# Kernel optimization log

Measured on AMD Instinct MI355X. Metric: run time of the kernel, lower is better.

Reference implementation:

```python
import jax, jax.numpy as jnp
import numpy as np

H, NH, HD = 1024, 16, 64
B, T, S = 2, 1024, 3
NOISE, STEP, TEMP, NSTEPS = 0.1, 0.01, 1.0, 5
LN_EPS = 1e-5


def setup_inputs() -> dict:
    key = jax.random.key(0)
    ks = jax.random.split(key, 9)
    return {
        "queries": jax.random.normal(ks[0], (B, NH, T, HD), jnp.float32),
        "keys": jax.random.normal(ks[1], (B, NH, T, HD), jnp.float32),
        "values": jax.random.normal(ks[2], (B, NH, T, HD), jnp.float32),
        "hidden_states": jax.random.normal(ks[3], (B, T, H), jnp.float32),
        "W1": jax.random.normal(ks[4], (H, H), jnp.float32) * 0.02,
        "b1": jnp.zeros((H,), jnp.float32),
        "ln_g": jnp.ones((H,), jnp.float32),
        "ln_b": jnp.zeros((H,), jnp.float32),
        "W2": jax.random.normal(ks[5], (H, H), jnp.float32) * 0.02,
        "b2": jnp.zeros((H,), jnp.float32),
        "hyp_noise": jax.random.normal(ks[6], (S, B, NH, T, HD), jnp.float32),
        "ref_noise": jax.random.normal(ks[7], (S, NSTEPS - 1, B, NH, T, HD), jnp.float32),
    }


def _attention_energy(q, k, v):
    # q: [S,B,H,T,D]; k,v: [B,H,T,D] -> energy [S,B]
    scores = jnp.einsum('sbhtd,bhud->sbhtu', q, k) / jnp.sqrt(jnp.float32(q.shape[-1]))
    attn = jax.nn.softmax(scores, axis=-1)
    out = jnp.einsum('sbhtu,bhud->sbhtd', attn, v)
    out_mag = jnp.linalg.norm(out, axis=-1).mean(axis=(2, 3))          # [S,B]
    entropy = -(attn * jnp.log(attn + 1e-8)).sum(axis=-1).mean(axis=(2, 3))
    align = (q * k[None]).sum(axis=-1).mean(axis=(2, 3))
    return out_mag - 0.1 * entropy - 0.05 * align


def reference(queries, keys, values, hidden_states, W1, b1, ln_g, ln_b, W2, b2,
              hyp_noise, ref_noise):
    # query_predictor: Linear -> LayerNorm -> ReLU -> Linear
    x = hidden_states @ W1.T + b1
    mu = x.mean(axis=-1, keepdims=True)
    var = ((x - mu) ** 2).mean(axis=-1, keepdims=True)
    x = (x - mu) / jnp.sqrt(var + LN_EPS) * ln_g + ln_b
    x = jax.nn.relu(x)
    ctx = x @ W2.T + b2                                   # [B,T,H]
    ctx = ctx.reshape(B, T, NH, HD).transpose(0, 2, 1, 3) # [B,NH,T,HD]

    # exploration hypotheses, refined jointly over the sample axis
    q = queries[None] + hyp_noise * NOISE                 # [S,B,NH,T,HD]
    for step in range(NSTEPS):
        q = q - STEP * (q - ctx[None])                    # PCN prediction-error update
        if step < NSTEPS - 1:
            q = q + ref_noise[:, step] * 0.01

    energies = _attention_energy(q, keys, values)         # [S,B]
    probs = jax.nn.softmax(-energies / TEMP, axis=0)      # [S,B]
    selected = jnp.einsum('sb,sbhtd->bhtd', probs, q)     # softmax-weighted mix
    return selected, keys, values
```

## Files before the change

kernel.cpp:

```cpp
#include <hip/hip_runtime.h>
#include <hip/hip_bf16.h>
#include <math.h>

#define NB 2
#define NHH 16
#define TT 1024
#define HDD 64
#define NSS 3
#define HH 1024
#define MMR 2048

typedef float f4 __attribute__((ext_vector_type(4)));
typedef short bf16x8 __attribute__((ext_vector_type(8)));
typedef unsigned short u16;
typedef u16 u16x4 __attribute__((ext_vector_type(4)));

__device__ inline u16 f2bf(float f) {
    union { float f; unsigned u; } v; v.f = f;
    unsigned r = (v.u + 0x7FFFu + ((v.u >> 16) & 1u)) >> 16;
    return (u16)r;
}
__device__ inline float bf2f(u16 u) {
    union { unsigned u; float f; } v; v.u = ((unsigned)u) << 16;
    return v.f;
}

__device__ inline float red16sum(float v) {
    v += __shfl_xor(v, 1);
    v += __shfl_xor(v, 2);
    v += __shfl_xor(v, 4);
    v += __shfl_xor(v, 8);
    return v;
}
__device__ inline float red64sum(float v) {
    v += __shfl_xor(v, 1);
    v += __shfl_xor(v, 2);
    v += __shfl_xor(v, 4);
    v += __shfl_xor(v, 8);
    v += __shfl_xor(v, 16);
    v += __shfl_xor(v, 32);
    return v;
}

__global__ __launch_bounds__(256) void k_cvt4(const float* __restrict__ s0, u16* __restrict__ d0,
                                              const float* __restrict__ s1, u16* __restrict__ d1,
                                              const float* __restrict__ s2, u16* __restrict__ d2,
                                              const float* __restrict__ s3, u16* __restrict__ d3,
                                              float* __restrict__ outk) {
    int b = blockIdx.x;
    if (b >= 4096) {
        int i = (b - 4096) * 256 + threadIdx.x;
        f4 v = ((const f4*)s3)[i];
        ((f4*)outk)[i] = v;
        u16x4 o;
        o[0] = f2bf(v[0] * 0.125f); o[1] = f2bf(v[1] * 0.125f);
        o[2] = f2bf(v[2] * 0.125f); o[3] = f2bf(v[3] * 0.125f);
        ((u16x4*)d3)[i] = o;
        return;
    }
    const float* s; u16* d; int base;
    if (b < 2048)      { s = s0; d = d0; base = 0; }
    else if (b < 3072) { s = s1; d = d1; base = 2048; }
    else               { s = s2; d = d2; base = 3072; }
    int i = (b - base) * 256 + threadIdx.x;
    f4 v = ((const f4*)s)[i];
    u16x4 o;
    o[0] = f2bf(v[0]); o[1] = f2bf(v[1]); o[2] = f2bf(v[2]); o[3] = f2bf(v[3]);
    ((u16x4*)d)[i] = o;
}

__global__ __launch_bounds__(256) void k_vtrans(const float* __restrict__ V,
                                                u16* __restrict__ Vt,
                                                float* __restrict__ outv) {
    __shared__ float tile[64][65];
    int bh = blockIdx.y, t0 = blockIdx.x * 64;
    int r = threadIdx.x >> 2, c0 = (threadIdx.x & 3) * 16;
    const float* vp = V + ((size_t)bh * TT + t0) * HDD;
#pragma unroll
    for (int j = 0; j < 16; j += 4) {
        f4 v = *(const f4*)(vp + r * HDD + c0 + j);
        tile[r][c0 + j + 0] = v[0]; tile[r][c0 + j + 1] = v[1];
        tile[r][c0 + j + 2] = v[2]; tile[r][c0 + j + 3] = v[3];
        *(f4*)(outv + ((size_t)bh * TT + t0 + r) * HDD + c0 + j) = v;
    }
    __syncthreads();
    int d = threadIdx.x >> 2, x0 = (threadIdx.x & 3) * 16;
    u16* op = Vt + ((size_t)bh * HDD + d) * TT + t0 + x0;
#pragma unroll
    for (int j = 0; j < 16; j += 4) {
        u16x4 o;
        o[0] = f2bf(tile[x0 + j + 0][d]); o[1] = f2bf(tile[x0 + j + 1][d]);
        o[2] = f2bf(tile[x0 + j + 2][d]); o[3] = f2bf(tile[x0 + j + 3][d]);
        *(u16x4*)(op + j) = o;
    }
}

template <int EPI>
__global__ __launch_bounds__(256) void k_gemm_bt(const u16* __restrict__ A,
                                                 const u16* __restrict__ Bm,
                                                 const float* __restrict__ bias,
                                                 float* __restrict__ out) {
    const int K = 1024, N = 1024;
    int w = threadIdx.x >> 6, l = threadIdx.x & 63, lr = l & 15, lg = l >> 4;
    int m0 = blockIdx.y * 64 + w * 16;
    int n0 = blockIdx.x * 64;
    const u16* ap = A + (size_t)(m0 + lr) * K + lg * 8;
    const u16* bp = Bm + (size_t)(n0 + lr) * K + lg * 8;
    f4 z4 = {0.f, 0.f, 0.f, 0.f};
    f4 acc[4] = {z4, z4, z4, z4};
#pragma unroll 2
    for (int kk = 0; kk < K; kk += 32) {
        bf16x8 a  = *(const bf16x8*)(ap + kk);
        bf16x8 b0 = *(const bf16x8*)(bp + kk);
        bf16x8 b1 = *(const bf16x8*)(bp + 16 * K + kk);
        bf16x8 b2 = *(const bf16x8*)(bp + 32 * K + kk);
        bf16x8 b3 = *(const bf16x8*)(bp + 48 * K + kk);
        acc[0] = __builtin_amdgcn_mfma_f32_16x16x32_bf16(a, b0, acc[0], 0, 0, 0);
        acc[1] = __builtin_amdgcn_mfma_f32_16x16x32_bf16(a, b1, acc[1], 0, 0, 0);
        acc[2] = __builtin_amdgcn_mfma_f32_16x16x32_bf16(a, b2, acc[2], 0, 0, 0);
        acc[3] = __builtin_amdgcn_mfma_f32_16x16x32_bf16(a, b3, acc[3], 0, 0, 0);
    }
#pragma unroll
    for (int cf = 0; cf < 4; ++cf) {
        int col = n0 + cf * 16 + lr;
        float bs = bias[col];
#pragma unroll
        for (int r = 0; r < 4; ++r) {
            int row = m0 + lg * 4 + r;
            float v = acc[cf][r] + bs;
            if (EPI == 0) {
                out[(size_t)row * N + col] = v;
            } else {
                int b = row >> 10, t = row & 1023, nh = col >> 6, hd = col & 63;
                out[(((size_t)(b * NHH + nh)) * TT + t) * HDD + hd] = v;
            }
        }
    }
}

__global__ __launch_bounds__(256) void k_lnrelu(const float* __restrict__ X,
                                                const float* __restrict__ g,
                                                const float* __restrict__ bta,
                                                u16* __restrict__ xr) {
    int row = blockIdx.x;
    f4 v = ((const f4*)(X + (size_t)row * HH))[threadIdx.x];
    float s = v[0] + v[1] + v[2] + v[3];
    float s2 = v[0] * v[0] + v[1] * v[1] + v[2] * v[2] + v[3] * v[3];
    s = red64sum(s);
    s2 = red64sum(s2);
    __shared__ float red[8];
    int w = threadIdx.x >> 6, l = threadIdx.x & 63;
    if (l == 0) { red[w] = s; red[w + 4] = s2; }
    __syncthreads();
    float S1 = red[0] + red[1] + red[2] + red[3];
    float S2 = red[4] + red[5] + red[6] + red[7];
    float mu = S1 * (1.0f / 1024.0f);
    float var = S2 * (1.0f / 1024.0f) - mu * mu;
    float rstd = rsqrtf(var + 1e-5f);
    f4 gv = ((const f4*)g)[threadIdx.x];
    f4 bv = ((const f4*)bta)[threadIdx.x];
    u16x4 o;
#pragma unroll
    for (int j = 0; j < 4; ++j) {
        float y = (v[j] - mu) * rstd * gv[j] + bv[j];
        y = fmaxf(y, 0.f);
        o[j] = f2bf(y);
    }
    ((u16x4*)(xr + (size_t)row * HH))[threadIdx.x] = o;
}

__global__ __launch_bounds__(256, 3) void k_attn(const float* __restrict__ que,
                                                 const float* __restrict__ ctx,
                                                 const float* __restrict__ hyp,
                                                 const float* __restrict__ rn,
                                                 const u16* __restrict__ Kb,
                                                 const u16* __restrict__ Vt,
                                                 u16* __restrict__ qq,
                                                 float* __restrict__ part) {
    int bi = blockIdx.x;
    int qt2 = bi & 7, h = (bi >> 3) & 15, sb = bi >> 7;
    int s = sb >> 1, b = sb & 1;
    int bh = b * NHH + h;
    int w = threadIdx.x >> 6, l = threadIdx.x & 63, lr = l & 15, lg = l >> 4;
    int t0 = qt2 * 128;
    f4 z4 = {0.f, 0.f, 0.f, 0.f};

    __shared__ u16 Ks[4096];
    __shared__ u16 Vs[4096];
    __shared__ u16 plds[8][1024];

    const float A5 = 0.9509900499f, CC = 1.0f - A5, CH = 0.1f * A5;
    const float C0 = 0.0096059601f, C1 = 0.0097029900f, C2 = 0.0098010000f, C3 = 0.0099f;
    const float* quep = que + ((size_t)bh * TT) * HDD;
    const float* ctxp = ctx + ((size_t)bh * TT) * HDD;
    const float* hypp = hyp + ((size_t)(sb * NHH + h) * TT) * HDD;
    const float* rn0p = rn + ((size_t)(((s * 4 + 0) * 2 + b) * NHH + h) * TT) * HDD;
    const float* rn1p = rn + ((size_t)(((s * 4 + 1) * 2 + b) * NHH + h) * TT) * HDD;
    const float* rn2p = rn + ((size_t)(((s * 4 + 2) * 2 + b) * NHH + h) * TT) * HDD;
    const float* rn3p = rn + ((size_t)(((s * 4 + 3) * 2 + b) * NHH + h) * TT) * HDD;
    u16* qqp = qq + ((size_t)(sb * NHH + h) * TT) * HDD;

    bf16x8 aq[2][2];
#pragma unroll
    for (int qr = 0; qr < 2; ++qr) {
        size_t ro = (size_t)(t0 + w * 32 + qr * 16 + lr) * HDD;
#pragma unroll
        for (int c = 0; c < 2; ++c) {
            int d0 = c * 32 + lg * 8;
            f4 va, vb;
#pragma unroll
            for (int half = 0; half < 2; ++half) {
                size_t off = ro + d0 + half * 4;
                f4 v = A5 * *(const f4*)(quep + off);
                v += CC * *(const f4*)(ctxp + off);
                v += CH * __builtin_nontemporal_load((const f4*)(hypp + off));
                v += C0 * __builtin_nontemporal_load((const f4*)(rn0p + off));
                v += C1 * __builtin_nontemporal_load((const f4*)(rn1p + off));
                v += C2 * __builtin_nontemporal_load((const f4*)(rn2p + off));
                v += C3 * __builtin_nontemporal_load((const f4*)(rn3p + off));
                if (half == 0) va = v; else vb = v;
            }
            union { bf16x8 f; u16 u[8]; int4 i4; } o;
#pragma unroll
            for (int j = 0; j < 4; ++j) { o.u[j] = f2bf(va[j]); o.u[4 + j] = f2bf(vb[j]); }
            aq[qr][c] = o.f;
            *(int4*)(qqp + ro + d0) = o.i4;
        }
    }

    const u16* kbase = Kb + (size_t)bh * TT * HDD;
    const u16* vbase = Vt + (size_t)bh * HDD * TT;
    int u0 = threadIdx.x, u1 = threadIdx.x + 256;
    const u16* kg0 = kbase + u0 * 8;
    const u16* kg1 = kbase + u1 * 8;
    const u16* vg0 = vbase + (size_t)(u0 >> 3) * TT + (u0 & 7) * 8;
    const u16* vg1 = vbase + (size_t)(u1 >> 3) * TT + (u1 & 7) * 8;
    int ko0 = (u0 >> 3) * 128 + (((u0 & 7) ^ ((u0 >> 3) & 7)) << 4);
    int ko1 = (u1 >> 3) * 128 + (((u1 & 7) ^ ((u1 >> 3) & 7)) << 4);
    char* KsB = (char*)Ks;
    char* VsB = (char*)Vs;

    int4 kr0 = *(const int4*)(kg0);
    int4 kr1 = *(const int4*)(kg1);
    int4 vr0 = *(const int4*)(vg0);
    int4 vr1 = *(const int4*)(vg1);

    f4 acco[2][4] = {{z4, z4, z4, z4}, {z4, z4, z4, z4}};
    float zrow[2][4] = {{0.f, 0.f, 0.f, 0.f}, {0.f, 0.f, 0.f, 0.f}};
    float wrow[2][4] = {{0.f, 0.f, 0.f, 0.f}, {0.f, 0.f, 0.f, 0.f}};

    for (int kt = 0; kt < 16; ++kt) {
        __syncthreads();
        *(int4*)(KsB + ko0) = kr0;
        *(int4*)(KsB + ko1) = kr1;
        *(int4*)(VsB + ko0) = vr0;
        *(int4*)(VsB + ko1) = vr1;
        if (kt < 15) {
            kr0 = *(const int4*)(kg0 + (kt + 1) * 4096);
            kr1 = *(const int4*)(kg1 + (kt + 1) * 4096);
            vr0 = *(const int4*)(vg0 + (kt + 1) * 64);
            vr1 = *(const int4*)(vg1 + (kt + 1) * 64);
        }
        __syncthreads();

        f4 sc[2][4];
#pragma unroll
        for (int cf = 0; cf < 4; ++cf) {
            int row = cf * 16 + lr, rs = row & 7;
            bf16x8 bk0 = *(const bf16x8*)(KsB + row * 128 + ((lg ^ rs) << 4));
            bf16x8 bk1 = *(const bf16x8*)(KsB + row * 128 + (((4 + lg) ^ rs) << 4));
            f4 t0a = __builtin_amdgcn_mfma_f32_16x16x32_bf16(aq[0][0], bk0, z4, 0, 0, 0);
            sc[0][cf] = __builtin_amdgcn_mfma_f32_16x16x32_bf16(aq[0][1], bk1, t0a, 0, 0, 0);
            f4 t1a = __builtin_amdgcn_mfma_f32_16x16x32_bf16(aq[1][0], bk0, z4, 0, 0, 0);
            sc[1][cf] = __builtin_amdgcn_mfma_f32_16x16x32_bf16(aq[1][1], bk1, t1a, 0, 0, 0);
        }

#pragma unroll
        for (int qr = 0; qr < 2; ++qr) {
            u16* pl = &plds[w * 2 + qr][0];
#pragma unroll
            for (int cf = 0; cf < 4; ++cf) {
#pragma unroll
                for (int r = 0; r < 4; ++r) {
                    float sv = sc[qr][cf][r];
                    float pe = __expf(sv);
                    zrow[qr][r] += pe;
                    wrow[qr][r] = fmaf(pe, sv, wrow[qr][r]);
                    int prow = lg * 4 + r;
                    pl[(prow * 64 + cf * 16 + lr) ^ ((prow & 7) << 3)] = f2bf(pe);
                }
            }
        }
        bf16x8 pa[2][2];
#pragma unroll
        for (int qr = 0; qr < 2; ++qr) {
            const u16* pl = &plds[w * 2 + qr][0];
            pa[qr][0] = *(const bf16x8*)&pl[(lr * 64 + lg * 8) ^ ((lr & 7) << 3)];
            pa[qr][1] = *(const bf16x8*)&pl[(lr * 64 + 32 + lg * 8) ^ ((lr & 7) << 3)];
        }
#pragma unroll
        for (int cf = 0; cf < 4; ++cf) {
            int row = cf * 16 + lr, rs = row & 7;
            bf16x8 bv0 = *(const bf16x8*)(VsB + row * 128 + ((lg ^ rs) << 4));
            bf16x8 bv1 = *(const bf16x8*)(VsB + row * 128 + (((4 + lg) ^ rs) << 4));
            acco[0][cf] = __builtin_amdgcn_mfma_f32_16x16x32_bf16(pa[0][0], bv0, acco[0][cf], 0, 0, 0);
            acco[0][cf] = __builtin_amdgcn_mfma_f32_16x16x32_bf16(pa[0][1], bv1, acco[0][cf], 0, 0, 0);
            acco[1][cf] = __builtin_amdgcn_mfma_f32_16x16x32_bf16(pa[1][0], bv0, acco[1][cf], 0, 0, 0);
            acco[1][cf] = __builtin_amdgcn_mfma_f32_16x16x32_bf16(pa[1][1], bv1, acco[1][cf], 0, 0, 0);
        }
    }

    float magw = 0.f, entw = 0.f;
#pragma unroll
    for (int qr = 0; qr < 2; ++qr) {
#pragma unroll
        for (int r = 0; r < 4; ++r) {
            float zz = red16sum(zrow[qr][r]);
            float ww = red16sum(wrow[qr][r]);
            float ssq = acco[qr][0][r] * acco[qr][0][r] + acco[qr][1][r] * acco[qr][1][r] +
                        acco[qr][2][r] * acco[qr][2][r] + acco[qr][3][r] * acco[qr][3][r];
            ssq = red16sum(ssq);
            float inv = 1.0f / zz;
            magw += sqrtf(ssq) * inv;
            entw += __logf(zz) - ww * inv;
        }
    }
    magw += __shfl_xor(magw, 16); magw += __shfl_xor(magw, 32);
    entw += __shfl_xor(entw, 16); entw += __shfl_xor(entw, 32);

    int arow = threadIdx.x >> 1, ah = (threadIdx.x & 1) * 32;
    const u16* qa = qqp + (size_t)(t0 + arow) * HDD + ah;
    const u16* ka = Kb + (((size_t)bh) * TT + t0 + arow) * HDD + ah;
    float al = 0.f;
#pragma unroll
    for (int j = 0; j < 32; j += 4) {
        u16x4 qv4 = *(const u16x4*)(qa + j);
        u16x4 kv4 = *(const u16x4*)(ka + j);
        al += bf2f(qv4[0]) * bf2f(kv4[0]) + bf2f(qv4[1]) * bf2f(kv4[1]) +
              bf2f(qv4[2]) * bf2f(kv4[2]) + bf2f(qv4[3]) * bf2f(kv4[3]);
    }
    al = red64sum(al) * 8.0f;

    __shared__ float red[4][3];
    if (l == 0) { red[w][0] = magw; red[w][1] = entw; red[w][2] = al; }
    __syncthreads();
    if (threadIdx.x == 0) {
        part[bi * 3 + 0] = red[0][0] + red[1][0] + red[2][0] + red[3][0];
        part[bi * 3 + 1] = red[0][1] + red[1][1] + red[2][1] + red[3][1];
        part[bi * 3 + 2] = red[0][2] + red[1][2] + red[2][2] + red[3][2];
    }
}

__global__ void k_finalize(const float* __restrict__ part, float* __restrict__ probs) {
    int w = threadIdx.x >> 6, l = threadIdx.x & 63;
    __shared__ float eng[6];
    if (w < 6) {
        float a0 = 0.f, a1 = 0.f, a2 = 0.f;
        for (int i = l; i < 128; i += 64) {
            const float* pp = part + (size_t)(w * 128 + i) * 3;
            a0 += pp[0]; a1 += pp[1]; a2 += pp[2];
        }
        a0 = red64sum(a0); a1 = red64sum(a1); a2 = red64sum(a2);
        if (l == 0) {
            const float inv = 1.0f / 16384.0f;
            eng[w] = a0 * inv - 0.1f * (a1 * inv) - 0.05f * (a2 * inv);
        }
    }
    __syncthreads();
    if (threadIdx.x < 2) {
        int b = threadIdx.x;
        float e0 = -eng[0 + b], e1 = -eng[2 + b], e2 = -eng[4 + b];
        float mx = fmaxf(e0, fmaxf(e1, e2));
        float x0 = __expf(e0 - mx), x1 = __expf(e1 - mx), x2 = __expf(e2 - mx);
        float inv = 1.0f / (x0 + x1 + x2);
        probs[0 + b] = x0 * inv;
        probs[2 + b] = x1 * inv;
        probs[4 + b] = x2 * inv;
    }
}

__global__ __launch_bounds__(256) void k_select(const u16* __restrict__ qq,
                                                const float* __restrict__ probs,
                                                float* __restrict__ out) {
    const int NQ4 = 524288;
    int i = blockIdx.x * 256 + threadIdx.x;
    int b = i >> 18;
    float p0 = probs[0 + b], p1 = probs[2 + b], p2 = probs[4 + b];
    u16x4 a0 = ((const u16x4*)qq)[i];
    u16x4 a1 = ((const u16x4*)qq)[NQ4 + i];
    u16x4 a2 = ((const u16x4*)qq)[2 * NQ4 + i];
    f4 v;
#pragma unroll
    for (int j = 0; j < 4; ++j)
        v[j] = p0 * bf2f(a0[j]) + p1 * bf2f(a1[j]) + p2 * bf2f(a2[j]);
    ((f4*)out)[i] = v;
}

extern "C" void kernel_launch(void* const* d_in, const int* in_sizes, int n_in,
                              void* d_out, int out_size, void* d_ws, size_t ws_size,
                              hipStream_t stream) {
    const float* queries = (const float*)d_in[0];
    const float* keys    = (const float*)d_in[1];
    const float* values  = (const float*)d_in[2];
    const float* hs      = (const float*)d_in[3];
    const float* W1      = (const float*)d_in[4];
    const float* b1      = (const float*)d_in[5];
    const float* ln_g    = (const float*)d_in[6];
    const float* ln_b    = (const float*)d_in[7];
    const float* W2      = (const float*)d_in[8];
    const float* b2      = (const float*)d_in[9];
    const float* hyp     = (const float*)d_in[10];
    const float* rn      = (const float*)d_in[11];
    float* out = (float*)d_out;
    char* ws = (char*)d_ws;

    const size_t MB = 1024ull * 1024ull;
    u16*   qq16 = (u16*)(ws);
    u16*   hs_b = (u16*)(ws + 0 * MB);
    u16*   w1_b = (u16*)(ws + 4 * MB);
    u16*   w2_b = (u16*)(ws + 6 * MB);
    float* X    = (float*)(ws + 8 * MB);
    u16*   xr   = (u16*)(ws + 16 * MB);
    float* ctx  = (float*)(ws + 24 * MB);
    u16*   k_b  = (u16*)(ws + 32 * MB);
    u16*   vt_b = (u16*)(ws + 36 * MB);
    float* part = (float*)(ws + 40 * MB);
    float* probs= (float*)(ws + 40 * MB + 65536);

    k_cvt4<<<6144, 256, 0, stream>>>(hs, hs_b, W1, w1_b, W2, w2_b, keys, k_b,
                                     out + 2097152);
    k_vtrans<<<dim3(16, 32), 256, 0, stream>>>(values, vt_b, out + 4194304);

    k_gemm_bt<0><<<dim3(16, 32), 256, 0, stream>>>(hs_b, w1_b, b1, X);
    k_lnrelu<<<2048, 256, 0, stream>>>(X, ln_g, ln_b, xr);
    k_gemm_bt<1><<<dim3(16, 32), 256, 0, stream>>>(xr, w2_b, b2, ctx);

    k_attn<<<768, 256, 0, stream>>>(queries, ctx, hyp, rn, k_b, vt_b, qq16, part);
    k_finalize<<<1, 384, 0, stream>>>(part, probs);
    k_select<<<2048, 256, 0, stream>>>(qq16, probs, out);
}
```

Measured before the change: 175.7 us.

## Compute transposed scores and repack P via cross-lane shuffles instead of LDS

The QK^T MFMA now swaps its operands so each lane holds scores for one query row across several keys. The exp'd probabilities are packed to bf16 with v_cvt_pk_bf16_f32 and rearranged into the PV A-operand layout with two rounds of __shfl_xor, replacing the per-warp LDS scratch round trip and freeing 16KB of shared memory. The per-row softmax sums are accumulated per lane and reduced once at the end, with the reduction logic adjusted to match. This removes LDS writes and reads and scalar bf16 conversions, at the cost of extra cross-lane shuffles and selects per tile.

After: 183.3 us. 1.04x slower.

```diff
diff --git a/kernel.cpp b/kernel.cpp
--- a/kernel.cpp
+++ b/kernel.cpp
@@ -182,12 +182,12 @@
     int s = sb >> 1, b = sb & 1;
     int bh = b * NHH + h;
     int w = threadIdx.x >> 6, l = threadIdx.x & 63, lr = l & 15, lg = l >> 4;
+    int b4 = (l >> 4) & 1, b5 = (l >> 5) & 1;
     int t0 = qt2 * 128;
     f4 z4 = {0.f, 0.f, 0.f, 0.f};
 
     __shared__ u16 Ks[4096];
     __shared__ u16 Vs[4096];
-    __shared__ u16 plds[8][1024];
 
     const float A5 = 0.9509900499f, CC = 1.0f - A5, CH = 0.1f * A5;
     const float C0 = 0.0096059601f, C1 = 0.0097029900f, C2 = 0.0098010000f, C3 = 0.0099f;
@@ -246,8 +246,8 @@
     int4 vr1 = *(const int4*)(vg1);
 
     f4 acco[2][4] = {{z4, z4, z4, z4}, {z4, z4, z4, z4}};
-    float zrow[2][4] = {{0.f, 0.f, 0.f, 0.f}, {0.f, 0.f, 0.f, 0.f}};
-    float wrow[2][4] = {{0.f, 0.f, 0.f, 0.f}, {0.f, 0.f, 0.f, 0.f}};
+    float zacc[2] = {0.f, 0.f};
+    float wacc[2] = {0.f, 0.f};
 
     for (int kt = 0; kt < 16; ++kt) {
         __syncthreads();
@@ -263,41 +263,64 @@
         }
         __syncthreads();
 
-        f4 sc[2][4];
+        f4 st[2][4];
 #pragma unroll
         for (int cf = 0; cf < 4; ++cf) {
             int row = cf * 16 + lr, rs = row & 7;
             bf16x8 bk0 = *(const bf16x8*)(KsB + row * 128 + ((lg ^ rs) << 4));
             bf16x8 bk1 = *(const bf16x8*)(KsB + row * 128 + (((4 + lg) ^ rs) << 4));
-            f4 t0a = __builtin_amdgcn_mfma_f32_16x16x32_bf16(aq[0][0], bk0, z4, 0, 0, 0);
-            sc[0][cf] = __builtin_amdgcn_mfma_f32_16x16x32_bf16(aq[0][1], bk1, t0a, 0, 0, 0);
-            f4 t1a = __builtin_amdgcn_mfma_f32_16x16x32_bf16(aq[1][0], bk0, z4, 0, 0, 0);
-            sc[1][cf] = __builtin_amdgcn_mfma_f32_16x16x32_bf16(aq[1][1], bk1, t1a, 0, 0, 0);
-        }
-
+            f4 t0a = __builtin_amdgcn_mfma_f32_16x16x32_bf16(bk0, aq[0][0], z4, 0, 0, 0);
+            st[0][cf] = __builtin_amdgcn_mfma_f32_16x16x32_bf16(bk1, aq[0][1], t0a, 0, 0, 0);
+            f4 t1a = __builtin_amdgcn_mfma_f32_16x16x32_bf16(bk0, aq[1][0], z4, 0, 0, 0);
+            st[1][cf] = __builtin_amdgcn_mfma_f32_16x16x32_bf16(bk1, aq[1][1], t1a, 0, 0, 0);
+        }
+
+        bf16x8 pa[2][2];
 #pragma unroll
         for (int qr = 0; qr < 2; ++qr) {
-            u16* pl = &plds[w * 2 + qr][0];
+            unsigned pk[4][2];
+            float zp = 0.f, wp = 0.f;
 #pragma unroll
             for (int cf = 0; cf < 4; ++cf) {
-#pragma unroll
-                for (int r = 0; r < 4; ++r) {
-                    float sv = sc[qr][cf][r];
-                    float pe = __expf(sv);
-                    zrow[qr][r] += pe;
-                    wrow[qr][r] = fmaf(pe, sv, wrow[qr][r]);
-                    int prow = lg * 4 + r;
-                    pl[(prow * 64 + cf * 16 + lr) ^ ((prow & 7) << 3)] = f2bf(pe);
+                float p0 = __expf(st[qr][cf][0]);
+                float p1 = __expf(st[qr][cf][1]);
+                float p2 = __expf(st[qr][cf][2]);
+                float p3 = __expf(st[qr][cf][3]);
+                zp += (p0 + p1) + (p2 + p3);
+                wp = fmaf(p0, st[qr][cf][0], wp);
+                wp = fmaf(p1, st[qr][cf][1], wp);
+                wp = fmaf(p2, st[qr][cf][2], wp);
+                wp = fmaf(p3, st[qr][cf][3], wp);
+                asm("v_cvt_pk_bf16_f32 %0, %1, %2" : "=v"(pk[cf][0]) : "v"(p0), "v"(p1));
+                asm("v_cvt_pk_bf16_f32 %0, %1, %2" : "=v"(pk[cf][1]) : "v"(p2), "v"(p3));
+            }
+            zacc[qr] += zp;
+            wacc[qr] += wp;
+            unsigned keep0[2][2], got0[2][2];
+#pragma unroll
+            for (int ch = 0; ch < 2; ++ch)
+#pragma unroll
+                for (int wi = 0; wi < 2; ++wi) {
+                    unsigned own  = b5 ? pk[2 * ch + 1][wi] : pk[2 * ch][wi];
+                    unsigned send = b5 ? pk[2 * ch][wi]     : pk[2 * ch + 1][wi];
+                    keep0[ch][wi] = own;
+                    got0[ch][wi]  = (unsigned)__shfl_xor((int)send, 32);
                 }
-            }
-        }
-        bf16x8 pa[2][2];
-#pragma unroll
-        for (int qr = 0; qr < 2; ++qr) {
-            const u16* pl = &plds[w * 2 + qr][0];
-            pa[qr][0] = *(const bf16x8*)&pl[(lr * 64 + lg * 8) ^ ((lr & 7) << 3)];
-            pa[qr][1] = *(const bf16x8*)&pl[(lr * 64 + 32 + lg * 8) ^ ((lr & 7) << 3)];
-        }
+            union { unsigned u[4]; bf16x8 f; } pc[2];
+#pragma unroll
+            for (int ch = 0; ch < 2; ++ch)
+#pragma unroll
+                for (int wi = 0; wi < 2; ++wi) {
+                    unsigned own2  = (b5 == b4) ? keep0[ch][wi] : got0[ch][wi];
+                    unsigned send2 = (b5 == b4) ? got0[ch][wi]  : keep0[ch][wi];
+                    unsigned got2  = (unsigned)__shfl_xor((int)send2, 16);
+                    pc[ch].u[wi]     = b4 ? got2 : own2;
+                    pc[ch].u[2 + wi] = b4 ? own2 : got2;
+                }
+            pa[qr][0] = pc[0].f;
+            pa[qr][1] = pc[1].f;
+        }
+
 #pragma unroll
         for (int cf = 0; cf < 4; ++cf) {
             int row = cf * 16 + lr, rs = row & 7;
@@ -310,23 +333,25 @@
         }
     }
 
-    float magw = 0.f, entw = 0.f;
+    float mag_lane = 0.f, ent_lane = 0.f;
 #pragma unroll
     for (int qr = 0; qr < 2; ++qr) {
+        float zf = zacc[qr];
+        zf += __shfl_xor(zf, 16); zf += __shfl_xor(zf, 32);
+        float wf = wacc[qr];
+        wf += __shfl_xor(wf, 16); wf += __shfl_xor(wf, 32);
+        ent_lane += __logf(zf) - wf / zf;
 #pragma unroll
         for (int r = 0; r < 4; ++r) {
-            float zz = red16sum(zrow[qr][r]);
-            float ww = red16sum(wrow[qr][r]);
             float ssq = acco[qr][0][r] * acco[qr][0][r] + acco[qr][1][r] * acco[qr][1][r] +
                         acco[qr][2][r] * acco[qr][2][r] + acco[qr][3][r] * acco[qr][3][r];
             ssq = red16sum(ssq);
-            float inv = 1.0f / zz;
-            magw += sqrtf(ssq) * inv;
-            entw += __logf(zz) - ww * inv;
-        }
-    }
-    magw += __shfl_xor(magw, 16); magw += __shfl_xor(magw, 32);
-    entw += __shfl_xor(entw, 16); entw += __shfl_xor(entw, 32);
+            float zq = __shfl(zf, lg * 4 + r);
+            mag_lane += sqrtf(ssq) / zq;
+        }
+    }
+    float magw = red64sum(mag_lane) * (1.0f / 16.0f);
+    float entw = red64sum(ent_lane) * 0.25f;
 
     int arow = threadIdx.x >> 1, ah = (threadIdx.x & 1) * 32;
     const u16* qa = qqp + (size_t)(t0 + arow) * HDD + ah;
```

## Fold query/ctx blend into GEMM epilogue, double-buffer K/V LDS, reuse diagonal scores

Applied to the files above, without the earlier changes.

The second GEMM epilogue now writes A5*queries + (1-A5)*ctx, so the attention kernel reads one fp32 tensor where it used to read two. K/V tiles are double-buffered in shared memory with a single barrier per iteration instead of two. The alignment term comes from the diagonal of the already computed QK score tiles, which removes the separate q·k reload pass. Block index mapping is reordered so concurrent blocks share the same s/qt2 across heads, with partials written to a remapped index. The cost is double the K/V LDS footprint, which may reduce occupancy at launch_bounds(256,3).

New measurement: 172.5 us. About the same (-1.8%).

```diff
diff --git a/kernel.cpp b/kernel.cpp
--- a/kernel.cpp
+++ b/kernel.cpp
@@ -99,6 +99,7 @@
 __global__ __launch_bounds__(256) void k_gemm_bt(const u16* __restrict__ A,
                                                  const u16* __restrict__ Bm,
                                                  const float* __restrict__ bias,
+                                                 const float* __restrict__ que,
                                                  float* __restrict__ out) {
     const int K = 1024, N = 1024;
     int w = threadIdx.x >> 6, l = threadIdx.x & 63, lr = l & 15, lg = l >> 4;
@@ -120,6 +121,7 @@
         acc[2] = __builtin_amdgcn_mfma_f32_16x16x32_bf16(a, b2, acc[2], 0, 0, 0);
         acc[3] = __builtin_amdgcn_mfma_f32_16x16x32_bf16(a, b3, acc[3], 0, 0, 0);
     }
+    const float A5 = 0.9509900499f, CC = 1.0f - A5;
 #pragma unroll
     for (int cf = 0; cf < 4; ++cf) {
         int col = n0 + cf * 16 + lr;
@@ -132,7 +134,8 @@
                 out[(size_t)row * N + col] = v;
             } else {
                 int b = row >> 10, t = row & 1023, nh = col >> 6, hd = col & 63;
-                out[(((size_t)(b * NHH + nh)) * TT + t) * HDD + hd] = v;
+                size_t oidx = (((size_t)(b * NHH + nh)) * TT + t) * HDD + hd;
+                out[oidx] = A5 * que[oidx] + CC * v;
             }
         }
     }
@@ -169,8 +172,7 @@
     ((u16x4*)(xr + (size_t)row * HH))[threadIdx.x] = o;
 }
 
-__global__ __launch_bounds__(256, 3) void k_attn(const float* __restrict__ que,
-                                                 const float* __restrict__ ctx,
+__global__ __launch_bounds__(256, 3) void k_attn(const float* __restrict__ basep_,
                                                  const float* __restrict__ hyp,
                                                  const float* __restrict__ rn,
                                                  const u16* __restrict__ Kb,
@@ -178,21 +180,23 @@
                                                  u16* __restrict__ qq,
                                                  float* __restrict__ part) {
     int bi = blockIdx.x;
-    int qt2 = bi & 7, h = (bi >> 3) & 15, sb = bi >> 7;
-    int s = sb >> 1, b = sb & 1;
+    int p_ = bi & 31, j_ = bi >> 5;
+    int h = p_ & 15, b = p_ >> 4;
+    int s = j_ >> 3, qt2 = j_ & 7;
+    int sb = s * 2 + b;
     int bh = b * NHH + h;
+    int pi = sb * 128 + h * 8 + qt2;
     int w = threadIdx.x >> 6, l = threadIdx.x & 63, lr = l & 15, lg = l >> 4;
     int t0 = qt2 * 128;
     f4 z4 = {0.f, 0.f, 0.f, 0.f};
 
-    __shared__ u16 Ks[4096];
-    __shared__ u16 Vs[4096];
+    __shared__ u16 Ks[2][4096];
+    __shared__ u16 Vs[2][4096];
     __shared__ u16 plds[8][1024];
 
-    const float A5 = 0.9509900499f, CC = 1.0f - A5, CH = 0.1f * A5;
+    const float CH = 0.1f * 0.9509900499f;
     const float C0 = 0.0096059601f, C1 = 0.0097029900f, C2 = 0.0098010000f, C3 = 0.0099f;
-    const float* quep = que + ((size_t)bh * TT) * HDD;
-    const float* ctxp = ctx + ((size_t)bh * TT) * HDD;
+    const float* basep = basep_ + ((size_t)bh * TT) * HDD;
     const float* hypp = hyp + ((size_t)(sb * NHH + h) * TT) * HDD;
     const float* rn0p = rn + ((size_t)(((s * 4 + 0) * 2 + b) * NHH + h) * TT) * HDD;
     const float* rn1p = rn + ((size_t)(((s * 4 + 1) * 2 + b) * NHH + h) * TT) * HDD;
@@ -211,8 +215,7 @@
 #pragma unroll
             for (int half = 0; half < 2; ++half) {
                 size_t off = ro + d0 + half * 4;
-                f4 v = A5 * *(const f4*)(quep + off);
-                v += CC * *(const f4*)(ctxp + off);
+                f4 v = *(const f4*)(basep + off);
                 v += CH * __builtin_nontemporal_load((const f4*)(hypp + off));
                 v += C0 * __builtin_nontemporal_load((const f4*)(rn0p + off));
                 v += C1 * __builtin_nontemporal_load((const f4*)(rn1p + off));
@@ -237,31 +240,33 @@
     const u16* vg1 = vbase + (size_t)(u1 >> 3) * TT + (u1 & 7) * 8;
     int ko0 = (u0 >> 3) * 128 + (((u0 & 7) ^ ((u0 >> 3) & 7)) << 4);
     int ko1 = (u1 >> 3) * 128 + (((u1 & 7) ^ ((u1 >> 3) & 7)) << 4);
-    char* KsB = (char*)Ks;
-    char* VsB = (char*)Vs;
 
     int4 kr0 = *(const int4*)(kg0);
     int4 kr1 = *(const int4*)(kg1);
     int4 vr0 = *(const int4*)(vg0);
     int4 vr1 = *(const int4*)(vg1);
+    *(int4*)((char*)Ks[0] + ko0) = kr0;
+    *(int4*)((char*)Ks[0] + ko1) = kr1;
+    *(int4*)((char*)Vs[0] + ko0) = vr0;
+    *(int4*)((char*)Vs[0] + ko1) = vr1;
+    __syncthreads();
 
     f4 acco[2][4] = {{z4, z4, z4, z4}, {z4, z4, z4, z4}};
     float zrow[2][4] = {{0.f, 0.f, 0.f, 0.f}, {0.f, 0.f, 0.f, 0.f}};
     float wrow[2][4] = {{0.f, 0.f, 0.f, 0.f}, {0.f, 0.f, 0.f, 0.f}};
+    float al_lane = 0.f;
+    int kdiag = qt2 * 2 + (w >> 1);
 
     for (int kt = 0; kt < 16; ++kt) {
-        __syncthreads();
-        *(int4*)(KsB + ko0) = kr0;
-        *(int4*)(KsB + ko1) = kr1;
-        *(int4*)(VsB + ko0) = vr0;
-        *(int4*)(VsB + ko1) = vr1;
+        int cur = kt & 1;
         if (kt < 15) {
             kr0 = *(const int4*)(kg0 + (kt + 1) * 4096);
             kr1 = *(const int4*)(kg1 + (kt + 1) * 4096);
             vr0 = *(const int4*)(vg0 + (kt + 1) * 64);
             vr1 = *(const int4*)(vg1 + (kt + 1) * 64);
         }
-        __syncthreads();
+        char* KsB = (char*)Ks[cur];
+        char* VsB = (char*)Vs[cur];
 
         f4 sc[2][4];
 #pragma unroll
@@ -273,6 +278,15 @@
             sc[0][cf] = __builtin_amdgcn_mfma_f32_16x16x32_bf16(aq[0][1], bk1, t0a, 0, 0, 0);
             f4 t1a = __builtin_amdgcn_mfma_f32_16x16x32_bf16(aq[1][0], bk0, z4, 0, 0, 0);
             sc[1][cf] = __builtin_amdgcn_mfma_f32_16x16x32_bf16(aq[1][1], bk1, t1a, 0, 0, 0);
+        }
+
+        if (kt == kdiag) {
+            f4 sd0 = (w & 1) ? sc[0][2] : sc[0][0];
+            f4 sd1 = (w & 1) ? sc[1][3] : sc[1][1];
+            int rr = lr & 3;
+            float e0 = rr == 0 ? sd0[0] : (rr == 1 ? sd0[1] : (rr == 2 ? sd0[2] : sd0[3]));
+            float e1 = rr == 0 ? sd1[0] : (rr == 1 ? sd1[1] : (rr == 2 ? sd1[2] : sd1[3]));
+            if (lg == (lr >> 2)) al_lane += (e0 + e1) * 8.0f;
         }
 
 #pragma unroll
@@ -308,6 +322,16 @@
             acco[1][cf] = __builtin_amdgcn_mfma_f32_16x16x32_bf16(pa[1][0], bv0, acco[1][cf], 0, 0, 0);
             acco[1][cf] = __builtin_amdgcn_mfma_f32_16x16x32_bf16(pa[1][1], bv1, acco[1][cf], 0, 0, 0);
         }
+
+        if (kt < 15) {
+            char* Kn = (char*)Ks[cur ^ 1];
+            char* Vn = (char*)Vs[cur ^ 1];
+            *(int4*)(Kn + ko0) = kr0;
+            *(int4*)(Kn + ko1) = kr1;
+            *(int4*)(Vn + ko0) = vr0;
+            *(int4*)(Vn + ko1) = vr1;
+        }
+        __syncthreads();
     }
 
     float magw = 0.f, entw = 0.f;
@@ -327,27 +351,15 @@
     }
     magw += __shfl_xor(magw, 16); magw += __shfl_xor(magw, 32);
     entw += __shfl_xor(entw, 16); entw += __shfl_xor(entw, 32);
-
-    int arow = threadIdx.x >> 1, ah = (threadIdx.x & 1) * 32;
-    const u16* qa = qqp + (size_t)(t0 + arow) * HDD + ah;
-    const u16* ka = Kb + (((size_t)bh) * TT + t0 + arow) * HDD + ah;
-    float al = 0.f;
-#pragma unroll
-    for (int j = 0; j < 32; j += 4) {
-        u16x4 qv4 = *(const u16x4*)(qa + j);
-        u16x4 kv4 = *(const u16x4*)(ka + j);
-        al += bf2f(qv4[0]) * bf2f(kv4[0]) + bf2f(qv4[1]) * bf2f(kv4[1]) +
-              bf2f(qv4[2]) * bf2f(kv4[2]) + bf2f(qv4[3]) * bf2f(kv4[3]);
-    }
-    al = red64sum(al) * 8.0f;
+    float al = red64sum(al_lane);
 
     __shared__ float red[4][3];
     if (l == 0) { red[w][0] = magw; red[w][1] = entw; red[w][2] = al; }
     __syncthreads();
     if (threadIdx.x == 0) {
-        part[bi * 3 + 0] = red[0][0] + red[1][0] + red[2][0] + red[3][0];
-        part[bi * 3 + 1] = red[0][1] + red[1][1] + red[2][1] + red[3][1];
-        part[bi * 3 + 2] = red[0][2] + red[1][2] + red[2][2] + red[3][2];
+        part[pi * 3 + 0] = red[0][0] + red[1][0] + red[2][0] + red[3][0];
+        part[pi * 3 + 1] = red[0][1] + red[1][1] + red[2][1] + red[3][1];
+        part[pi * 3 + 2] = red[0][2] + red[1][2] + red[2][2] + red[3][2];
     }
 }
 
@@ -421,7 +433,7 @@
     u16*   w2_b = (u16*)(ws + 6 * MB);
     float* X    = (float*)(ws + 8 * MB);
     u16*   xr   = (u16*)(ws + 16 * MB);
-    float* ctx  = (float*)(ws + 24 * MB);
+    float* base = (float*)(ws + 24 * MB);
     u16*   k_b  = (u16*)(ws + 32 * MB);
     u16*   vt_b = (u16*)(ws + 36 * MB);
     float* part = (float*)(ws + 40 * MB);
@@ -431,11 +443,11 @@
                                      out + 2097152);
     k_vtrans<<<dim3(16, 32), 256, 0, stream>>>(values, vt_b, out + 4194304);
 
-    k_gemm_bt<0><<<dim3(16, 32), 256, 0, stream>>>(hs_b, w1_b, b1, X);
+    k_gemm_bt<0><<<dim3(16, 32), 256, 0, stream>>>(hs_b, w1_b, b1, nullptr, X);
     k_lnrelu<<<2048, 256, 0, stream>>>(X, ln_g, ln_b, xr);
-    k_gemm_bt<1><<<dim3(16, 32), 256, 0, stream>>>(xr, w2_b, b2, ctx);
-
-    k_attn<<<768, 256, 0, stream>>>(queries, ctx, hyp, rn, k_b, vt_b, qq16, part);
+    k_gemm_bt<1><<<dim3(16, 32), 256, 0, stream>>>(xr, w2_b, b2, queries, base);
+
+    k_attn<<<768, 256, 0, stream>>>(base, hyp, rn, k_b, vt_b, qq16, part);
     k_finalize<<<1, 384, 0, stream>>>(part, probs);
     k_select<<<2048, 256, 0, stream>>>(qq16, probs, out);
 }
```
